# Kernel optimization log

Hardware: AMD Instinct MI355X
Metric: run time of the kernel (lower is better)

The kernel has to match this reference:

```python
import jax, jax.numpy as jnp
import numpy as np

D_MODEL = 1024
NUM_HEADS = 16
GROUPS = 4
HEADS_PER_GROUP = NUM_HEADS // GROUPS
D_K = D_MODEL // NUM_HEADS
B, S = 2, 2048


def setup_inputs() -> dict:
    key = jax.random.key(0)
    ks = jax.random.split(key, 10)
    sc = 0.02
    return {
        "x": jax.random.normal(ks[0], (B, S, D_MODEL), dtype=jnp.float32),
        "W_Q": jax.random.normal(ks[1], (D_MODEL, D_MODEL), dtype=jnp.float32) * sc,
        "b_Q": jnp.zeros((D_MODEL,), dtype=jnp.float32),
        "W_K": jax.random.normal(ks[2], (GROUPS, D_MODEL, D_K), dtype=jnp.float32) * sc,
        "b_K": jnp.zeros((GROUPS, D_K), dtype=jnp.float32),
        "W_V": jax.random.normal(ks[3], (GROUPS, D_MODEL, D_K), dtype=jnp.float32) * sc,
        "b_V": jnp.zeros((GROUPS, D_K), dtype=jnp.float32),
        "W_O": jax.random.normal(ks[4], (D_MODEL, D_MODEL), dtype=jnp.float32) * sc,
        "b_O": jnp.zeros((D_MODEL,), dtype=jnp.float32),
    }


def reference(x, W_Q, b_Q, W_K, b_K, W_V, b_V, W_O, b_O):
    b, s, _ = x.shape
    # Q: [b, s, d_model] -> [b, groups, heads_per_group, s, d_k]
    Q = (x @ W_Q + b_Q).reshape(b, s, NUM_HEADS, D_K).transpose(0, 2, 1, 3)
    Q = Q.reshape(b, GROUPS, HEADS_PER_GROUP, s, D_K)
    # Shared K/V per group: [b, groups, s, d_k]
    K = jnp.einsum('bsd,gdk->bgsk', x, W_K) + b_K[None, :, None, :]
    V = jnp.einsum('bsd,gdk->bgsk', x, W_V) + b_V[None, :, None, :]
    # scores: [b, groups, heads_per_group, s, s]
    scores = jnp.einsum('bghsk,bgtk->bghst', Q, K) / jnp.sqrt(jnp.float32(D_K))
    attn = jax.nn.softmax(scores, axis=-1)
    # context: [b, groups, heads_per_group, s, d_k] -> [b, s, d_model]
    ctx = jnp.einsum('bghst,bgtk->bghsk', attn, V)
    ctx = ctx.reshape(b, NUM_HEADS, s, D_K).transpose(0, 2, 1, 3).reshape(b, s, D_MODEL)
    return ctx @ W_O + b_O
```

## Files before the change

### kernel.cpp

```cpp
#include <hip/hip_runtime.h>
#include <cstdint>
#include <cstddef>

typedef short bf16x8 __attribute__((ext_vector_type(8)));
typedef float f32x4 __attribute__((ext_vector_type(4)));

#define DM 1024
#define NHEADS 16
#define NGROUPS 4
#define DK 64
#define BATCH 2
#define SEQ 2048
#define MROWS 4096

#define QB_ELEMS   ((size_t)BATCH*NHEADS*SEQ*DK)
#define KB_ELEMS   ((size_t)BATCH*NGROUPS*SEQ*DK)
#define VT_ELEMS   KB_ELEMS
#define XC_ELEMS   ((size_t)MROWS*DM)
#define WQKV_ELEMS ((size_t)1536*DM)
#define WO_ELEMS   ((size_t)DM*DM)

#define SCL_Q 0.180336880f

__device__ __forceinline__ ushort f2bf(float f) {
    union { float f; uint32_t u; } a; a.f = f;
    uint32_t u = a.u;
    return (ushort)((u + 0x7FFFu + ((u >> 16) & 1u)) >> 16);
}

__device__ __forceinline__ void gll16(const void* g, void* l) {
    __builtin_amdgcn_global_load_lds((const __attribute__((address_space(1))) void*)g,
                                     (__attribute__((address_space(3))) void*)l, 16, 0, 0);
}

__global__ __launch_bounds__(256) void gqa_prep_kernel(
        const float* __restrict__ x,
        const float* __restrict__ WQ, const float* __restrict__ WK,
        const float* __restrict__ WV, const float* __restrict__ WO,
        const float* __restrict__ bQ, const float* __restrict__ bK,
        const float* __restrict__ bV,
        ushort* __restrict__ xbf, ushort* __restrict__ WqkvT,
        ushort* __restrict__ WoT, float* __restrict__ bcat)
{
    __shared__ float tl[64][65];
    const int bid = blockIdx.x, tid = threadIdx.x;
    if (bid < 640) {
        const float* src; ushort* dst; int src_ld; int r0, c0;
        if (bid < 256) {
            src = WQ; src_ld = 1024; dst = WqkvT;
            r0 = (bid >> 4) * 64; c0 = (bid & 15) * 64;
        } else if (bid < 512) {
            int t = bid - 256;
            src = WO; src_ld = 1024; dst = WoT;
            r0 = (t >> 4) * 64; c0 = (t & 15) * 64;
        } else if (bid < 576) {
            int t = bid - 512; int g = t >> 4;
            src = WK + (size_t)g * 1024 * 64; src_ld = 64;
            dst = WqkvT + (size_t)(1024 + g * 64) * 1024;
            r0 = (t & 15) * 64; c0 = 0;
        } else {
            int t = bid - 576; int g = t >> 4;
            src = WV + (size_t)g * 1024 * 64; src_ld = 64;
            dst = WqkvT + (size_t)(1280 + g * 64) * 1024;
            r0 = (t & 15) * 64; c0 = 0;
        }
        const int rr = tid >> 4, cc = (tid & 15) * 4;
#pragma unroll
        for (int p = 0; p < 4; p++) {
            int r = rr + p * 16;
            float4 v = *(const float4*)(src + (size_t)(r0 + r) * src_ld + c0 + cc);
            tl[cc + 0][r] = v.x; tl[cc + 1][r] = v.y;
            tl[cc + 2][r] = v.z; tl[cc + 3][r] = v.w;
        }
        __syncthreads();
#pragma unroll
        for (int p = 0; p < 4; p++) {
            int c = rr + p * 16;
            ushort4 o;
            o.x = f2bf(tl[c][cc + 0]); o.y = f2bf(tl[c][cc + 1]);
            o.z = f2bf(tl[c][cc + 2]); o.w = f2bf(tl[c][cc + 3]);
            *(ushort4*)(dst + (size_t)(c0 + c) * 1024 + r0 + cc) = o;
        }
    } else if (bid < 896) {
        int cid = bid - 640;
        const float* xs = x + (size_t)cid * 16384;
        ushort* xd = xbf + (size_t)cid * 16384;
#pragma unroll
        for (int p = 0; p < 16; p++) {
            float4 v = *(const float4*)(xs + p * 1024 + tid * 4);
            ushort4 o = { f2bf(v.x), f2bf(v.y), f2bf(v.z), f2bf(v.w) };
            *(ushort4*)(xd + p * 1024 + tid * 4) = o;
        }
    } else {
        for (int i = tid; i < 1536; i += 256) {
            float v = (i < 1024) ? bQ[i] : (i < 1280 ? bK[i - 1024] : bV[i - 1280]);
            bcat[i] = v;
        }
    }
}

template<bool QKV_EPI>
__global__ __launch_bounds__(256, 2) void gqa_gemm_kernel(
        const ushort* __restrict__ A, const ushort* __restrict__ BT,
        const float* __restrict__ bias, float* __restrict__ outF,
        ushort* __restrict__ Qb, ushort* __restrict__ Kb, ushort* __restrict__ Vtg)
{
    __shared__ ushort As[2][128 * 64];
    __shared__ ushort Bs[2][64 * 64];
    const int tid = threadIdx.x;
    const int bm = blockIdx.x, bn = blockIdx.y;
    const int wave = tid >> 6, lane = tid & 63;
    const int wm = (wave & 1) * 64, wn = (wave >> 1) * 32;
    const int lr = lane & 15, lq = lane >> 4;
    const int swz = lr & 7;

    const ushort* srcA[4]; int dstA[4];
    const ushort* srcB[2]; int dstB[2];
#pragma unroll
    for (int p = 0; p < 4; p++) {
        int slot = p * 256 + tid;
        int row = slot >> 3, cb = (slot & 7) ^ (row & 7);
        srcA[p] = A + (size_t)(bm * 128 + row) * 1024 + cb * 8;
        dstA[p] = p * 2048 + wave * 512;
    }
#pragma unroll
    for (int p = 0; p < 2; p++) {
        int slot = p * 256 + tid;
        int row = slot >> 3, cb = (slot & 7) ^ (row & 7);
        srcB[p] = BT + (size_t)(bn * 64 + row) * 1024 + cb * 8;
        dstB[p] = p * 2048 + wave * 512;
    }

    f32x4 acc[4][2];
#pragma unroll
    for (int i = 0; i < 4; i++)
#pragma unroll
        for (int j = 0; j < 2; j++) acc[i][j] = (f32x4){0.f, 0.f, 0.f, 0.f};

#pragma unroll
    for (int p = 0; p < 4; p++) gll16(srcA[p], &As[0][dstA[p]]);
#pragma unroll
    for (int p = 0; p < 2; p++) gll16(srcB[p], &Bs[0][dstB[p]]);

    for (int kt = 0; kt < 16; kt++) {
        __syncthreads();
        if (kt < 15) {
            int buf = (kt + 1) & 1, ko = (kt + 1) * 64;
#pragma unroll
            for (int p = 0; p < 4; p++) gll16(srcA[p] + ko, &As[buf][dstA[p]]);
#pragma unroll
            for (int p = 0; p < 2; p++) gll16(srcB[p] + ko, &Bs[buf][dstB[p]]);
        }
        const ushort* as = As[kt & 1];
        const ushort* bs = Bs[kt & 1];
        bf16x8 af[2][4], bfr[2][2];
#pragma unroll
        for (int kh = 0; kh < 2; kh++) {
#pragma unroll
            for (int i = 0; i < 4; i++)
                af[kh][i] = *(const bf16x8*)&as[(wm + i * 16 + lr) * 64 + ((kh * 4 + lq) ^ swz) * 8];
#pragma unroll
            for (int j = 0; j < 2; j++)
                bfr[kh][j] = *(const bf16x8*)&bs[(wn + j * 16 + lr) * 64 + ((kh * 4 + lq) ^ swz) * 8];
        }
#pragma unroll
        for (int kh = 0; kh < 2; kh++)
#pragma unroll
            for (int i = 0; i < 4; i++)
#pragma unroll
                for (int j = 0; j < 2; j++)
                    acc[i][j] = __builtin_amdgcn_mfma_f32_16x16x32_bf16(af[kh][i], bfr[kh][j], acc[i][j], 0, 0, 0);
    }

#pragma unroll
    for (int i = 0; i < 4; i++) {
        int mg = bm * 128 + wm + i * 16 + lq * 4;
        int b = mg >> 11, s = mg & 2047;
#pragma unroll
        for (int j = 0; j < 2; j++) {
            int cg = bn * 64 + wn + j * 16 + lr;
            float bv = bias[cg];
            if constexpr (QKV_EPI) {
                int d = cg & 63;
                if (cg < 1024) {
                    int h = cg >> 6;
                    ushort* dst = Qb + ((size_t)(b * NHEADS + h) * SEQ + s) * DK + d;
#pragma unroll
                    for (int r = 0; r < 4; r++)
                        dst[r * DK] = f2bf((acc[i][j][r] + bv) * SCL_Q);
                } else if (cg < 1280) {
                    int g = (cg - 1024) >> 6;
                    ushort* dst = Kb + ((size_t)(b * NGROUPS + g) * SEQ + s) * DK + d;
#pragma unroll
                    for (int r = 0; r < 4; r++) dst[r * DK] = f2bf(acc[i][j][r] + bv);
                } else {
                    int g = (cg - 1280) >> 6;
                    int s4 = s >> 2, kg = s4 & 7;
                    int col = ((s4 >> 3) << 5) + (((((kg & 3) << 1) | (kg >> 2))) << 2);
                    ushort4 pk;
                    pk.x = f2bf(acc[i][j][0] + bv); pk.y = f2bf(acc[i][j][1] + bv);
                    pk.z = f2bf(acc[i][j][2] + bv); pk.w = f2bf(acc[i][j][3] + bv);
                    *(ushort4*)(Vtg + ((size_t)(b * NGROUPS + g) * DK + d) * SEQ + col) = pk;
                }
            } else {
#pragma unroll
                for (int r = 0; r < 4; r++)
                    outF[(size_t)(mg + r) * DM + cg] = acc[i][j][r] + bv;
            }
        }
    }
}

__global__ __launch_bounds__(256, 2) void gqa_attn_kernel(
        const ushort* __restrict__ Qb, const ushort* __restrict__ Kb,
        const ushort* __restrict__ Vtg, ushort* __restrict__ ctx)
{
    __shared__ ushort Ks[2][64 * 64];
    __shared__ ushort Vs[2][64 * 64];

    const int tid = threadIdx.x, wave = tid >> 6, lane = tid & 63;
    const int lr = lane & 15, lq = lane >> 4;
    const int swz = lr & 7;
    const int blk = blockIdx.x;
    const int qt = blk & 15, bh = blk >> 4;
    const int b = bh >> 4, hg = bh & 15, g = hg >> 2;

    const ushort* Qh = Qb  + (size_t)(b * NHEADS  + hg) * SEQ * DK;
    const ushort* Kg = Kb  + (size_t)(b * NGROUPS + g)  * SEQ * DK;
    const ushort* Vg = Vtg + (size_t)(b * NGROUPS + g)  * DK * SEQ;

    const int s0 = qt * 128 + wave * 32;

    bf16x8 qf[2][2];
#pragma unroll
    for (int qs = 0; qs < 2; qs++)
#pragma unroll
        for (int h = 0; h < 2; h++)
            qf[qs][h] = *(const bf16x8*)(Qh + (size_t)(s0 + qs * 16 + lr) * DK + h * 32 + lq * 8);

    const ushort* srcK[2]; const ushort* srcV[2]; int dstOff[2];
#pragma unroll
    for (int p = 0; p < 2; p++) {
        int slot = p * 256 + tid;
        int row = slot >> 3, cb = (slot & 7) ^ (row & 7);
        srcK[p] = Kg + (size_t)row * DK + cb * 8;
        srcV[p] = Vg + (size_t)row * SEQ + cb * 8;
        dstOff[p] = p * 2048 + wave * 512;
    }

    f32x4 of[2][4];
#pragma unroll
    for (int qs = 0; qs < 2; qs++)
#pragma unroll
        for (int j = 0; j < 4; j++) of[qs][j] = (f32x4){0.f, 0.f, 0.f, 0.f};
    f32x4 accL[2] = {(f32x4){0.f,0.f,0.f,0.f}, (f32x4){0.f,0.f,0.f,0.f}};

    bf16x8 ones;
#pragma unroll
    for (int i = 0; i < 8; i++) ones[i] = (short)0x3F80;

#pragma unroll
    for (int p = 0; p < 2; p++) {
        gll16(srcK[p], &Ks[0][dstOff[p]]);
        gll16(srcV[p], &Vs[0][dstOff[p]]);
    }

    for (int it = 0; it < 32; it++) {
        __syncthreads();
        if (it < 31) {
            int buf = (it + 1) & 1, t0 = (it + 1) * 64;
#pragma unroll
            for (int p = 0; p < 2; p++) {
                gll16(srcK[p] + (size_t)t0 * DK, &Ks[buf][dstOff[p]]);
                gll16(srcV[p] + t0, &Vs[buf][dstOff[p]]);
            }
        }
        const ushort* ks = Ks[it & 1];
        const ushort* vs = Vs[it & 1];

        bf16x8 kf[4][2];
#pragma unroll
        for (int nt = 0; nt < 4; nt++)
#pragma unroll
            for (int h = 0; h < 2; h++)
                kf[nt][h] = *(const bf16x8*)&ks[((nt * 16 + lr) * 8 + ((h * 4 + lq) ^ swz)) * 8];

        f32x4 sc[2][4];
#pragma unroll
        for (int qs = 0; qs < 2; qs++)
#pragma unroll
            for (int nt = 0; nt < 4; nt++) {
                f32x4 s = (f32x4){0.f, 0.f, 0.f, 0.f};
                s = __builtin_amdgcn_mfma_f32_16x16x32_bf16(kf[nt][0], qf[qs][0], s, 0, 0, 0);
                s = __builtin_amdgcn_mfma_f32_16x16x32_bf16(kf[nt][1], qf[qs][1], s, 0, 0, 0);
                sc[qs][nt] = s;
            }

        union PF { bf16x8 v; uint32_t w[4]; };
        PF pf[2][2];
#pragma unroll
        for (int qs = 0; qs < 2; qs++) {
#pragma unroll
            for (int nt = 0; nt < 4; nt++) {
                union { float f; uint32_t u; } e0, e1, e2, e3;
                e0.f = __builtin_amdgcn_exp2f(sc[qs][nt][0]);
                e1.f = __builtin_amdgcn_exp2f(sc[qs][nt][1]);
                e2.f = __builtin_amdgcn_exp2f(sc[qs][nt][2]);
                e3.f = __builtin_amdgcn_exp2f(sc[qs][nt][3]);
                pf[qs][nt >> 1].w[(nt & 1) * 2 + 0] = __builtin_amdgcn_perm(e1.u, e0.u, 0x07060302u);
                pf[qs][nt >> 1].w[(nt & 1) * 2 + 1] = __builtin_amdgcn_perm(e3.u, e2.u, 0x07060302u);
            }
            accL[qs] = __builtin_amdgcn_mfma_f32_16x16x32_bf16(ones, pf[qs][0].v, accL[qs], 0, 0, 0);
            accL[qs] = __builtin_amdgcn_mfma_f32_16x16x32_bf16(ones, pf[qs][1].v, accL[qs], 0, 0, 0);
        }

        bf16x8 vf[4][2];
#pragma unroll
        for (int j = 0; j < 4; j++)
#pragma unroll
            for (int kh = 0; kh < 2; kh++)
                vf[j][kh] = *(const bf16x8*)&vs[((j * 16 + lr) * 8 + ((kh * 4 + lq) ^ swz)) * 8];

#pragma unroll
        for (int qs = 0; qs < 2; qs++)
#pragma unroll
            for (int j = 0; j < 4; j++) {
                of[qs][j] = __builtin_amdgcn_mfma_f32_16x16x32_bf16(vf[j][0], pf[qs][0].v, of[qs][j], 0, 0, 0);
                of[qs][j] = __builtin_amdgcn_mfma_f32_16x16x32_bf16(vf[j][1], pf[qs][1].v, of[qs][j], 0, 0, 0);
            }
    }

    float inv[2];
    inv[0] = 1.0f / accL[0][0];
    inv[1] = 1.0f / accL[1][0];

    ushort* cbp = ctx + (size_t)b * SEQ * DM;
#pragma unroll
    for (int qs = 0; qs < 2; qs++) {
        int s = s0 + qs * 16 + lr;
#pragma unroll
        for (int j = 0; j < 4; j++) {
            ushort4 o;
            o.x = f2bf(of[qs][j][0] * inv[qs]);
            o.y = f2bf(of[qs][j][1] * inv[qs]);
            o.z = f2bf(of[qs][j][2] * inv[qs]);
            o.w = f2bf(of[qs][j][3] * inv[qs]);
            *(ushort4*)(cbp + (size_t)s * DM + hg * 64 + j * 16 + lq * 4) = o;
        }
    }
}

extern "C" void kernel_launch(void* const* d_in, const int* in_sizes, int n_in,
                              void* d_out, int out_size, void* d_ws, size_t ws_size,
                              hipStream_t stream) {
    const float* x  = (const float*)d_in[0];
    const float* WQ = (const float*)d_in[1];
    const float* bQ = (const float*)d_in[2];
    const float* WK = (const float*)d_in[3];
    const float* bK = (const float*)d_in[4];
    const float* WV = (const float*)d_in[5];
    const float* bV = (const float*)d_in[6];
    const float* WO = (const float*)d_in[7];
    const float* bO = (const float*)d_in[8];

    ushort* Qb    = (ushort*)d_ws;
    ushort* Kb    = Qb + QB_ELEMS;
    ushort* Vtg   = Kb + KB_ELEMS;
    ushort* xc    = Vtg + VT_ELEMS;
    ushort* WqkvT = xc + XC_ELEMS;
    ushort* WoT   = WqkvT + WQKV_ELEMS;
    float*  bcat  = (float*)(WoT + WO_ELEMS);

    gqa_prep_kernel<<<897, 256, 0, stream>>>(x, WQ, WK, WV, WO, bQ, bK, bV,
                                             xc, WqkvT, WoT, bcat);
    gqa_gemm_kernel<true><<<dim3(32, 24), 256, 0, stream>>>(
        xc, WqkvT, bcat, nullptr, Qb, Kb, Vtg);
    gqa_attn_kernel<<<512, 256, 0, stream>>>(Qb, Kb, Vtg, xc);
    gqa_gemm_kernel<false><<<dim3(32, 16), 256, 0, stream>>>(
        xc, WoT, bO, (float*)d_out, nullptr, nullptr, nullptr);
}
```

Measured before the change: 162.9 us.

## Split attention KV tile across wave pairs and remap blocks for XCD locality

The attention kernel now has each wave handle 64 query rows and half of each 64-key tile. The two partial outputs and row sums are combined through shared memory at the end, which halves per-wave K/V fragment loads relative to query work but adds a final reduction and more accumulator registers. Both the GEMM and attention launches use a 1D grid with block-index remapping, so blocks sharing A rows, or sharing the same group's K/V, land on the same XCD for L2 reuse. The GEMM launch bound is raised to 3 blocks per CU, which may raise register pressure.

```diff
diff --git a/kernel.cpp b/kernel.cpp
--- a/kernel.cpp
+++ b/kernel.cpp
@@ -99,8 +99,8 @@
     }
 }
 
-template<bool QKV_EPI>
-__global__ __launch_bounds__(256, 2) void gqa_gemm_kernel(
+template<bool QKV_EPI, int BN>
+__global__ __launch_bounds__(256, 3) void gqa_gemm_kernel(
         const ushort* __restrict__ A, const ushort* __restrict__ BT,
         const float* __restrict__ bias, float* __restrict__ outF,
         ushort* __restrict__ Qb, ushort* __restrict__ Kb, ushort* __restrict__ Vtg)
@@ -108,7 +108,10 @@
     __shared__ ushort As[2][128 * 64];
     __shared__ ushort Bs[2][64 * 64];
     const int tid = threadIdx.x;
-    const int bm = blockIdx.x, bn = blockIdx.y;
+    const int i = blockIdx.x;
+    const int xcd = i & 7, slot = i >> 3;
+    const int bm = (slot / BN) * 8 + xcd;
+    const int bn = slot % BN;
     const int wave = tid >> 6, lane = tid & 63;
     const int wm = (wave & 1) * 64, wn = (wave >> 1) * 32;
     const int lr = lane & 15, lq = lane >> 4;
@@ -118,24 +121,24 @@
     const ushort* srcB[2]; int dstB[2];
 #pragma unroll
     for (int p = 0; p < 4; p++) {
-        int slot = p * 256 + tid;
-        int row = slot >> 3, cb = (slot & 7) ^ (row & 7);
+        int slt = p * 256 + tid;
+        int row = slt >> 3, cb = (slt & 7) ^ (row & 7);
         srcA[p] = A + (size_t)(bm * 128 + row) * 1024 + cb * 8;
         dstA[p] = p * 2048 + wave * 512;
     }
 #pragma unroll
     for (int p = 0; p < 2; p++) {
-        int slot = p * 256 + tid;
-        int row = slot >> 3, cb = (slot & 7) ^ (row & 7);
+        int slt = p * 256 + tid;
+        int row = slt >> 3, cb = (slt & 7) ^ (row & 7);
         srcB[p] = BT + (size_t)(bn * 64 + row) * 1024 + cb * 8;
         dstB[p] = p * 2048 + wave * 512;
     }
 
     f32x4 acc[4][2];
 #pragma unroll
-    for (int i = 0; i < 4; i++)
-#pragma unroll
-        for (int j = 0; j < 2; j++) acc[i][j] = (f32x4){0.f, 0.f, 0.f, 0.f};
+    for (int ii = 0; ii < 4; ii++)
+#pragma unroll
+        for (int j = 0; j < 2; j++) acc[ii][j] = (f32x4){0.f, 0.f, 0.f, 0.f};
 
 #pragma unroll
     for (int p = 0; p < 4; p++) gll16(srcA[p], &As[0][dstA[p]]);
@@ -157,8 +160,8 @@
 #pragma unroll
         for (int kh = 0; kh < 2; kh++) {
 #pragma unroll
-            for (int i = 0; i < 4; i++)
-                af[kh][i] = *(const bf16x8*)&as[(wm + i * 16 + lr) * 64 + ((kh * 4 + lq) ^ swz) * 8];
+            for (int ii = 0; ii < 4; ii++)
+                af[kh][ii] = *(const bf16x8*)&as[(wm + ii * 16 + lr) * 64 + ((kh * 4 + lq) ^ swz) * 8];
 #pragma unroll
             for (int j = 0; j < 2; j++)
                 bfr[kh][j] = *(const bf16x8*)&bs[(wn + j * 16 + lr) * 64 + ((kh * 4 + lq) ^ swz) * 8];
@@ -166,15 +169,15 @@
 #pragma unroll
         for (int kh = 0; kh < 2; kh++)
 #pragma unroll
-            for (int i = 0; i < 4; i++)
+            for (int ii = 0; ii < 4; ii++)
 #pragma unroll
                 for (int j = 0; j < 2; j++)
-                    acc[i][j] = __builtin_amdgcn_mfma_f32_16x16x32_bf16(af[kh][i], bfr[kh][j], acc[i][j], 0, 0, 0);
-    }
-
-#pragma unroll
-    for (int i = 0; i < 4; i++) {
-        int mg = bm * 128 + wm + i * 16 + lq * 4;
+                    acc[ii][j] = __builtin_amdgcn_mfma_f32_16x16x32_bf16(af[kh][ii], bfr[kh][j], acc[ii][j], 0, 0, 0);
+    }
+
+#pragma unroll
+    for (int ii = 0; ii < 4; ii++) {
+        int mg = bm * 128 + wm + ii * 16 + lq * 4;
         int b = mg >> 11, s = mg & 2047;
 #pragma unroll
         for (int j = 0; j < 2; j++) {
@@ -187,25 +190,25 @@
                     ushort* dst = Qb + ((size_t)(b * NHEADS + h) * SEQ + s) * DK + d;
 #pragma unroll
                     for (int r = 0; r < 4; r++)
-                        dst[r * DK] = f2bf((acc[i][j][r] + bv) * SCL_Q);
+                        dst[r * DK] = f2bf((acc[ii][j][r] + bv) * SCL_Q);
                 } else if (cg < 1280) {
                     int g = (cg - 1024) >> 6;
                     ushort* dst = Kb + ((size_t)(b * NGROUPS + g) * SEQ + s) * DK + d;
 #pragma unroll
-                    for (int r = 0; r < 4; r++) dst[r * DK] = f2bf(acc[i][j][r] + bv);
+                    for (int r = 0; r < 4; r++) dst[r * DK] = f2bf(acc[ii][j][r] + bv);
                 } else {
                     int g = (cg - 1280) >> 6;
                     int s4 = s >> 2, kg = s4 & 7;
                     int col = ((s4 >> 3) << 5) + (((((kg & 3) << 1) | (kg >> 2))) << 2);
                     ushort4 pk;
-                    pk.x = f2bf(acc[i][j][0] + bv); pk.y = f2bf(acc[i][j][1] + bv);
-                    pk.z = f2bf(acc[i][j][2] + bv); pk.w = f2bf(acc[i][j][3] + bv);
+                    pk.x = f2bf(acc[ii][j][0] + bv); pk.y = f2bf(acc[ii][j][1] + bv);
+                    pk.z = f2bf(acc[ii][j][2] + bv); pk.w = f2bf(acc[ii][j][3] + bv);
                     *(ushort4*)(Vtg + ((size_t)(b * NGROUPS + g) * DK + d) * SEQ + col) = pk;
                 }
             } else {
 #pragma unroll
                 for (int r = 0; r < 4; r++)
-                    outF[(size_t)(mg + r) * DM + cg] = acc[i][j][r] + bv;
+                    outF[(size_t)(mg + r) * DM + cg] = acc[ii][j][r] + bv;
             }
         }
     }
@@ -215,54 +218,59 @@
         const ushort* __restrict__ Qb, const ushort* __restrict__ Kb,
         const ushort* __restrict__ Vtg, ushort* __restrict__ ctx)
 {
-    __shared__ ushort Ks[2][64 * 64];
-    __shared__ ushort Vs[2][64 * 64];
+    __shared__ ushort smem[2][2][64 * 64];
+    __shared__ float accX[2][4][16];
 
     const int tid = threadIdx.x, wave = tid >> 6, lane = tid & 63;
     const int lr = lane & 15, lq = lane >> 4;
     const int swz = lr & 7;
-    const int blk = blockIdx.x;
-    const int qt = blk & 15, bh = blk >> 4;
-    const int b = bh >> 4, hg = bh & 15, g = hg >> 2;
+    const int wq = wave & 1, wt = wave >> 1;
+    const int i = blockIdx.x;
+    const int bg = i & 7, s2 = i >> 3;
+    const int qt = s2 & 15, h = s2 >> 4;
+    const int b = bg >> 2, g = bg & 3, hg = g * 4 + h;
 
     const ushort* Qh = Qb  + (size_t)(b * NHEADS  + hg) * SEQ * DK;
     const ushort* Kg = Kb  + (size_t)(b * NGROUPS + g)  * SEQ * DK;
     const ushort* Vg = Vtg + (size_t)(b * NGROUPS + g)  * DK * SEQ;
 
-    const int s0 = qt * 128 + wave * 32;
-
-    bf16x8 qf[2][2];
-#pragma unroll
-    for (int qs = 0; qs < 2; qs++)
-#pragma unroll
-        for (int h = 0; h < 2; h++)
-            qf[qs][h] = *(const bf16x8*)(Qh + (size_t)(s0 + qs * 16 + lr) * DK + h * 32 + lq * 8);
+    const int s0 = qt * 128 + wq * 64;
+    const int tb = wt * 32;
+
+    bf16x8 qf[4][2];
+#pragma unroll
+    for (int qs = 0; qs < 4; qs++)
+#pragma unroll
+        for (int kh = 0; kh < 2; kh++)
+            qf[qs][kh] = *(const bf16x8*)(Qh + (size_t)(s0 + qs * 16 + lr) * DK + kh * 32 + lq * 8);
 
     const ushort* srcK[2]; const ushort* srcV[2]; int dstOff[2];
 #pragma unroll
     for (int p = 0; p < 2; p++) {
-        int slot = p * 256 + tid;
-        int row = slot >> 3, cb = (slot & 7) ^ (row & 7);
+        int slt = p * 256 + tid;
+        int row = slt >> 3, cb = (slt & 7) ^ (row & 7);
         srcK[p] = Kg + (size_t)row * DK + cb * 8;
         srcV[p] = Vg + (size_t)row * SEQ + cb * 8;
         dstOff[p] = p * 2048 + wave * 512;
     }
 
-    f32x4 of[2][4];
-#pragma unroll
-    for (int qs = 0; qs < 2; qs++)
+    f32x4 of[4][4];
+#pragma unroll
+    for (int qs = 0; qs < 4; qs++)
 #pragma unroll
         for (int j = 0; j < 4; j++) of[qs][j] = (f32x4){0.f, 0.f, 0.f, 0.f};
-    f32x4 accL[2] = {(f32x4){0.f,0.f,0.f,0.f}, (f32x4){0.f,0.f,0.f,0.f}};
+    f32x4 accL[4];
+#pragma unroll
+    for (int qs = 0; qs < 4; qs++) accL[qs] = (f32x4){0.f, 0.f, 0.f, 0.f};
 
     bf16x8 ones;
 #pragma unroll
-    for (int i = 0; i < 8; i++) ones[i] = (short)0x3F80;
+    for (int k = 0; k < 8; k++) ones[k] = (short)0x3F80;
 
 #pragma unroll
     for (int p = 0; p < 2; p++) {
-        gll16(srcK[p], &Ks[0][dstOff[p]]);
-        gll16(srcV[p], &Vs[0][dstOff[p]]);
+        gll16(srcK[p], &smem[0][0][dstOff[p]]);
+        gll16(srcV[p], &smem[1][0][dstOff[p]]);
     }
 
     for (int it = 0; it < 32; it++) {
@@ -271,25 +279,30 @@
             int buf = (it + 1) & 1, t0 = (it + 1) * 64;
 #pragma unroll
             for (int p = 0; p < 2; p++) {
-                gll16(srcK[p] + (size_t)t0 * DK, &Ks[buf][dstOff[p]]);
-                gll16(srcV[p] + t0, &Vs[buf][dstOff[p]]);
+                gll16(srcK[p] + (size_t)t0 * DK, &smem[0][buf][dstOff[p]]);
+                gll16(srcV[p] + t0, &smem[1][buf][dstOff[p]]);
             }
         }
-        const ushort* ks = Ks[it & 1];
-        const ushort* vs = Vs[it & 1];
-
-        bf16x8 kf[4][2];
-#pragma unroll
-        for (int nt = 0; nt < 4; nt++)
-#pragma unroll
-            for (int h = 0; h < 2; h++)
-                kf[nt][h] = *(const bf16x8*)&ks[((nt * 16 + lr) * 8 + ((h * 4 + lq) ^ swz)) * 8];
-
-        f32x4 sc[2][4];
-#pragma unroll
-        for (int qs = 0; qs < 2; qs++)
-#pragma unroll
-            for (int nt = 0; nt < 4; nt++) {
+        const ushort* ks = smem[0][it & 1];
+        const ushort* vs = smem[1][it & 1];
+
+        bf16x8 kf[2][2];
+#pragma unroll
+        for (int nt = 0; nt < 2; nt++)
+#pragma unroll
+            for (int kh = 0; kh < 2; kh++)
+                kf[nt][kh] = *(const bf16x8*)&ks[((tb + nt * 16 + lr) * 8 + ((kh * 4 + lq) ^ swz)) * 8];
+
+        bf16x8 vf[4];
+#pragma unroll
+        for (int j = 0; j < 4; j++)
+            vf[j] = *(const bf16x8*)&vs[((j * 16 + lr) * 8 + ((wt * 4 + lq) ^ swz)) * 8];
+
+        f32x4 sc[4][2];
+#pragma unroll
+        for (int qs = 0; qs < 4; qs++)
+#pragma unroll
+            for (int nt = 0; nt < 2; nt++) {
                 f32x4 s = (f32x4){0.f, 0.f, 0.f, 0.f};
                 s = __builtin_amdgcn_mfma_f32_16x16x32_bf16(kf[nt][0], qf[qs][0], s, 0, 0, 0);
                 s = __builtin_amdgcn_mfma_f32_16x16x32_bf16(kf[nt][1], qf[qs][1], s, 0, 0, 0);
@@ -297,55 +310,64 @@
             }
 
         union PF { bf16x8 v; uint32_t w[4]; };
-        PF pf[2][2];
-#pragma unroll
-        for (int qs = 0; qs < 2; qs++) {
-#pragma unroll
-            for (int nt = 0; nt < 4; nt++) {
+        PF pf[4];
+#pragma unroll
+        for (int qs = 0; qs < 4; qs++) {
+#pragma unroll
+            for (int nt = 0; nt < 2; nt++) {
                 union { float f; uint32_t u; } e0, e1, e2, e3;
                 e0.f = __builtin_amdgcn_exp2f(sc[qs][nt][0]);
                 e1.f = __builtin_amdgcn_exp2f(sc[qs][nt][1]);
                 e2.f = __builtin_amdgcn_exp2f(sc[qs][nt][2]);
                 e3.f = __builtin_amdgcn_exp2f(sc[qs][nt][3]);
-                pf[qs][nt >> 1].w[(nt & 1) * 2 + 0] = __builtin_amdgcn_perm(e1.u, e0.u, 0x07060302u);
-                pf[qs][nt >> 1].w[(nt & 1) * 2 + 1] = __builtin_amdgcn_perm(e3.u, e2.u, 0x07060302u);
+                pf[qs].w[nt * 2 + 0] = __builtin_amdgcn_perm(e1.u, e0.u, 0x07060302u);
+                pf[qs].w[nt * 2 + 1] = __builtin_amdgcn_perm(e3.u, e2.u, 0x07060302u);
             }
-            accL[qs] = __builtin_amdgcn_mfma_f32_16x16x32_bf16(ones, pf[qs][0].v, accL[qs], 0, 0, 0);
-            accL[qs] = __builtin_amdgcn_mfma_f32_16x16x32_bf16(ones, pf[qs][1].v, accL[qs], 0, 0, 0);
-        }
-
-        bf16x8 vf[4][2];
-#pragma unroll
-        for (int j = 0; j < 4; j++)
-#pragma unroll
-            for (int kh = 0; kh < 2; kh++)
-                vf[j][kh] = *(const bf16x8*)&vs[((j * 16 + lr) * 8 + ((kh * 4 + lq) ^ swz)) * 8];
-
-#pragma unroll
-        for (int qs = 0; qs < 2; qs++)
+            accL[qs] = __builtin_amdgcn_mfma_f32_16x16x32_bf16(ones, pf[qs].v, accL[qs], 0, 0, 0);
+        }
+
+#pragma unroll
+        for (int qs = 0; qs < 4; qs++)
+#pragma unroll
+            for (int j = 0; j < 4; j++)
+                of[qs][j] = __builtin_amdgcn_mfma_f32_16x16x32_bf16(vf[j], pf[qs].v, of[qs][j], 0, 0, 0);
+    }
+
+    __syncthreads();
+    float* comb = (float*)&smem[0][0][0];
+    if (wt == 1) {
+        float* cw = comb + wq * 4096;
+#pragma unroll
+        for (int qs = 0; qs < 4; qs++)
+#pragma unroll
+            for (int j = 0; j < 4; j++)
+                *(f32x4*)&cw[(qs * 4 + j) * 256 + lane * 4] = of[qs][j];
+        if (lq == 0) {
+#pragma unroll
+            for (int qs = 0; qs < 4; qs++) accX[wq][qs][lr] = accL[qs][0];
+        }
+    }
+    __syncthreads();
+    if (wt == 0) {
+        const float* cw = comb + wq * 4096;
+        float inv[4];
+#pragma unroll
+        for (int qs = 0; qs < 4; qs++)
+            inv[qs] = 1.0f / (accL[qs][0] + accX[wq][qs][lr]);
+        ushort* cbp = ctx + (size_t)b * SEQ * DM;
+#pragma unroll
+        for (int qs = 0; qs < 4; qs++) {
+            int s = s0 + qs * 16 + lr;
 #pragma unroll
             for (int j = 0; j < 4; j++) {
-                of[qs][j] = __builtin_amdgcn_mfma_f32_16x16x32_bf16(vf[j][0], pf[qs][0].v, of[qs][j], 0, 0, 0);
-                of[qs][j] = __builtin_amdgcn_mfma_f32_16x16x32_bf16(vf[j][1], pf[qs][1].v, of[qs][j], 0, 0, 0);
+                f32x4 o2 = of[qs][j] + *(const f32x4*)&cw[(qs * 4 + j) * 256 + lane * 4];
+                ushort4 o;
+                o.x = f2bf(o2[0] * inv[qs]);
+                o.y = f2bf(o2[1] * inv[qs]);
+                o.z = f2bf(o2[2] * inv[qs]);
+                o.w = f2bf(o2[3] * inv[qs]);
+                *(ushort4*)(cbp + (size_t)s * DM + hg * 64 + j * 16 + lq * 4) = o;
             }
-    }
-
-    float inv[2];
-    inv[0] = 1.0f / accL[0][0];
-    inv[1] = 1.0f / accL[1][0];
-
-    ushort* cbp = ctx + (size_t)b * SEQ * DM;
-#pragma unroll
-    for (int qs = 0; qs < 2; qs++) {
-        int s = s0 + qs * 16 + lr;
-#pragma unroll
-        for (int j = 0; j < 4; j++) {
-            ushort4 o;
-            o.x = f2bf(of[qs][j][0] * inv[qs]);
-            o.y = f2bf(of[qs][j][1] * inv[qs]);
-            o.z = f2bf(of[qs][j][2] * inv[qs]);
-            o.w = f2bf(of[qs][j][3] * inv[qs]);
-            *(ushort4*)(cbp + (size_t)s * DM + hg * 64 + j * 16 + lq * 4) = o;
         }
     }
 }
@@ -373,9 +395,9 @@
 
     gqa_prep_kernel<<<897, 256, 0, stream>>>(x, WQ, WK, WV, WO, bQ, bK, bV,
                                              xc, WqkvT, WoT, bcat);
-    gqa_gemm_kernel<true><<<dim3(32, 24), 256, 0, stream>>>(
+    gqa_gemm_kernel<true, 24><<<768, 256, 0, stream>>>(
         xc, WqkvT, bcat, nullptr, Qb, Kb, Vtg);
     gqa_attn_kernel<<<512, 256, 0, stream>>>(Qb, Kb, Vtg, xc);
-    gqa_gemm_kernel<false><<<dim3(32, 16), 256, 0, stream>>>(
+    gqa_gemm_kernel<false, 16><<<512, 256, 0, stream>>>(
         xc, WoT, bO, (float*)d_out, nullptr, nullptr, nullptr);
 }
```

After: 163.3 us. Within noise of the previous version (+0.2%).
